# Performance work log

Hardware: AMD Instinct MI355X
Metric: run time of the kernel (lower is better)

The kernel has to match this reference:

```python
import jax, jax.numpy as jnp
import numpy as np

B, L, D = 16, 512, 128   # batch of sequences, seq len, input_dim
BN_EPS = 1e-5
TEMP = 1.0


def setup_inputs() -> dict:
    key = jax.random.key(0)
    ks = jax.random.split(key, 5)
    ids = jax.random.randint(ks[0], (B, L), 0, 50000)            # item ids per (seq, pos)
    log_mask = jnp.ones((B, L), dtype=jnp.int32)                 # all positions valid (static N)
    x1 = jax.random.normal(ks[1], (B * L, D), dtype=jnp.float32)
    x2 = jax.random.normal(ks[2], (B * L, D), dtype=jnp.float32)
    w1 = jax.random.normal(ks[3], (2 * D, D), dtype=jnp.float32) * 0.05  # torch Linear: [out, in]
    b1 = jnp.zeros((2 * D,), jnp.float32)
    w2 = jax.random.normal(ks[4], (D, 2 * D), dtype=jnp.float32) * 0.05
    b2 = jnp.zeros((D,), jnp.float32)
    gamma = jnp.ones((D,), jnp.float32)   # BatchNorm1d affine weight
    beta = jnp.zeros((D,), jnp.float32)   # BatchNorm1d affine bias
    return dict(ids=ids, log_mask=log_mask, x1=x1, x2=x2,
                w1=w1, b1=b1, w2=w2, b2=b2, gamma=gamma, beta=beta)


def _embed(x, w1, b1, w2, b2, gamma, beta):
    """linear1 -> relu -> linear2 -> BatchNorm1d (train-mode batch stats) -> L2 normalize."""
    h = jax.nn.relu(x @ w1.T + b1)
    y = h @ w2.T + b2
    mu = y.mean(axis=0)
    var = ((y - mu) ** 2).mean(axis=0)          # biased var, as torch BN uses for normalization
    y = (y - mu) * jax.lax.rsqrt(var + BN_EPS) * gamma + beta
    return y / jnp.linalg.norm(y, axis=1, keepdims=True)


def reference(ids, log_mask, x1, x2, w1, b1, w2, b2, gamma, beta):
    # log_mask is all-nonzero in this setup, so the gather by nonzero indices is the identity.
    nb, nl = ids.shape
    N = x1.shape[0]                      # = nb * nl valid anchors
    ids_f = ids.reshape(-1)
    seq = jnp.repeat(jnp.arange(nb), nl)  # seq_indexs: which sequence each row belongs to

    z1 = _embed(x1, w1, b1, w2, b2, gamma, beta)
    z2 = _embed(x2, w1, b1, w2, b2, gamma, beta)
    S = z1 @ z2.T                        # [N, N] cosine similarity (rows already unit-norm)

    idx = jnp.arange(N)
    ids_next = jnp.roll(ids_f, -1)
    seq_next = jnp.roll(seq, -1)
    # two-positive branch: i < N-1 and same sequence as the next row
    two = (idx < N - 1) & (seq == seq_next)            # [N] bool

    diag = jnp.diagonal(S)                             # cos(anchor_i, input2_i)
    s_next = S[idx, (idx + 1) % N]                     # cos(anchor_i, input2_{i+1})

    cols = idx[None, :]
    neg1 = ids_f[None, :] != ids_f[:, None]                                # single-pos negatives
    neg2 = neg1 & (ids_f[None, :] != ids_next[:, None]) & (seq[None, :] != seq[:, None])
    mask = jnp.where(two[:, None], neg2, neg1)
    # add the positives (self, and i+1 in the two-positive branch)
    mask = mask | (cols == idx[:, None]) | (two[:, None] & (cols == idx[:, None] + 1))

    denom = jnp.sum(jnp.where(mask, jnp.exp(S / TEMP), 0.0), axis=1)       # [N]
    pos_sum = diag + jnp.where(two, s_next, 0.0)
    n_pos = 1.0 + two.astype(S.dtype)

    inner = -(pos_sum / TEMP - jnp.log(denom)) / n_pos
    return jnp.sum(inner) / N
```

## Files before the change

### kernel.cpp

```cpp
#include <hip/hip_runtime.h>

#define N_TOT 8192
#define SEQ_L 512
#define D 128
#define NCHUNK 16
#define CHUNK (N_TOT / NCHUNK)
#define NJT (CHUNK / 64)
#define LOG2E 1.4426950408889634f
#define LN2   0.6931471805599453f

using bf16x8  = __attribute__((ext_vector_type(8))) short;
using f32x4   = __attribute__((ext_vector_type(4))) float;

static __device__ __forceinline__ unsigned short f2bf(float f) {
    unsigned int u = __float_as_uint(f);
    u = (u + 0x7FFFu + ((u >> 16) & 1u)) >> 16;
    return (unsigned short)u;
}
static __device__ __forceinline__ float bf2f(unsigned short h) {
    return __uint_as_float(((unsigned int)h) << 16);
}
static __device__ __forceinline__ float dot8(bf16x8 a, bf16x8 b) {
    float s = 0.f;
    #pragma unroll
    for (int k = 0; k < 8; ++k)
        s = fmaf(bf2f((unsigned short)a[k]), bf2f((unsigned short)b[k]), s);
    return s;
}

__global__ __launch_bounds__(256) void convert_w_kernel(
    const float* __restrict__ w1, const float* __restrict__ w2,
    unsigned short* __restrict__ w1b, unsigned short* __restrict__ w2b)
{
    int idx = blockIdx.x * 256 + threadIdx.x;
    const float* src = (idx < 8192) ? w1 : w2;
    unsigned short* dst = (idx < 8192) ? w1b : w2b;
    int off = ((idx < 8192) ? idx : idx - 8192) * 4;
    float4 v = *(const float4*)(src + off);
    ushort4 o;
    o.x = f2bf(v.x); o.y = f2bf(v.y); o.z = f2bf(v.z); o.w = f2bf(v.w);
    *(ushort4*)(dst + off) = o;
}

__global__ __launch_bounds__(256) void mlp_mfma_kernel(
    const float* __restrict__ x1, const float* __restrict__ x2,
    const unsigned short* __restrict__ w1b, const float* __restrict__ b1,
    const unsigned short* __restrict__ w2b, const float* __restrict__ b2,
    unsigned short* __restrict__ z1, unsigned short* __restrict__ z2,
    float* __restrict__ part_s, float* __restrict__ part_ss)
{
    __shared__ unsigned short hsh[32][264];
    const int t = threadIdx.x;
    const int w = t >> 6;
    const int lane = t & 63;
    const int g = lane >> 4;
    const int c16 = lane & 15;
    const int tensor = blockIdx.x >> 8;
    const int blk = blockIdx.x & 255;
    const int r0 = blk * 32;
    const float* __restrict__ x = tensor ? x2 : x1;
    unsigned short* __restrict__ z = tensor ? z2 : z1;

    bf16x8 af[2][4];
    #pragma unroll
    for (int rf = 0; rf < 2; ++rf)
        #pragma unroll
        for (int ks = 0; ks < 4; ++ks) {
            const float* xp = x + (size_t)(r0 + rf * 16 + c16) * D + ks * 32 + g * 8;
            float4 u0 = *(const float4*)xp;
            float4 u1 = *(const float4*)(xp + 4);
            bf16x8 a;
            a[0] = f2bf(u0.x); a[1] = f2bf(u0.y); a[2] = f2bf(u0.z); a[3] = f2bf(u0.w);
            a[4] = f2bf(u1.x); a[5] = f2bf(u1.y); a[6] = f2bf(u1.z); a[7] = f2bf(u1.w);
            af[rf][ks] = a;
        }
    f32x4 acc1[2][4] = {};
    #pragma unroll
    for (int ks = 0; ks < 4; ++ks)
        #pragma unroll
        for (int nf = 0; nf < 4; ++nf) {
            int n = w * 64 + nf * 16 + c16;
            bf16x8 b = *(const bf16x8*)(w1b + (size_t)n * D + ks * 32 + g * 8);
            #pragma unroll
            for (int rf = 0; rf < 2; ++rf)
                acc1[rf][nf] = __builtin_amdgcn_mfma_f32_16x16x32_bf16(af[rf][ks], b, acc1[rf][nf], 0, 0, 0);
        }
    #pragma unroll
    for (int nf = 0; nf < 4; ++nf) {
        float bb = b1[w * 64 + nf * 16 + c16];
        #pragma unroll
        for (int rf = 0; rf < 2; ++rf)
            #pragma unroll
            for (int r = 0; r < 4; ++r)
                hsh[rf * 16 + g * 4 + r][w * 64 + nf * 16 + c16] = f2bf(fmaxf(acc1[rf][nf][r] + bb, 0.f));
    }
    __syncthreads();

    f32x4 acc2[2][2] = {};
    #pragma unroll
    for (int ks = 0; ks < 8; ++ks) {
        bf16x8 a0 = *(const bf16x8*)(&hsh[c16][ks * 32 + g * 8]);
        bf16x8 a1 = *(const bf16x8*)(&hsh[16 + c16][ks * 32 + g * 8]);
        #pragma unroll
        for (int nf = 0; nf < 2; ++nf) {
            int n = w * 32 + nf * 16 + c16;
            bf16x8 b = *(const bf16x8*)(w2b + (size_t)n * 256 + ks * 32 + g * 8);
            acc2[0][nf] = __builtin_amdgcn_mfma_f32_16x16x32_bf16(a0, b, acc2[0][nf], 0, 0, 0);
            acc2[1][nf] = __builtin_amdgcn_mfma_f32_16x16x32_bf16(a1, b, acc2[1][nf], 0, 0, 0);
        }
    }

    #pragma unroll
    for (int nf = 0; nf < 2; ++nf) {
        int col = w * 32 + nf * 16 + c16;
        float bb = b2[col];
        float s = 0.f, ss = 0.f;
        #pragma unroll
        for (int rf = 0; rf < 2; ++rf)
            #pragma unroll
            for (int r = 0; r < 4; ++r) {
                float v = acc2[rf][nf][r] + bb;
                z[(size_t)(r0 + rf * 16 + g * 4 + r) * D + col] = f2bf(v);
                s += v; ss += v * v;
            }
        s  += __shfl_xor(s, 16);  s  += __shfl_xor(s, 32);
        ss += __shfl_xor(ss, 16); ss += __shfl_xor(ss, 32);
        if (g == 0) {
            part_s [((size_t)tensor * 256 + blk) * D + col] = s;
            part_ss[((size_t)tensor * 256 + blk) * D + col] = ss;
        }
    }
}

__global__ __launch_bounds__(256) void bn_reduce_kernel(
    const float* __restrict__ part_s, const float* __restrict__ part_ss,
    const float* __restrict__ gamma,
    float* __restrict__ mu, float* __restrict__ sc)
{
    const int t = threadIdx.x;
    const int tensor = blockIdx.x >> 7;
    const int col = blockIdx.x & 127;
    float s  = part_s [((size_t)tensor * 256 + t) * D + col];
    float ss = part_ss[((size_t)tensor * 256 + t) * D + col];
    #pragma unroll
    for (int m = 32; m; m >>= 1) { s += __shfl_xor(s, m); ss += __shfl_xor(ss, m); }
    __shared__ float rs[4], rss[4];
    if ((t & 63) == 0) { rs[t >> 6] = s; rss[t >> 6] = ss; }
    __syncthreads();
    if (t == 0) {
        float S = rs[0] + rs[1] + rs[2] + rs[3];
        float SS = rss[0] + rss[1] + rss[2] + rss[3];
        float m = S / (float)N_TOT;
        float var = SS / (float)N_TOT - m * m;
        mu[tensor * D + col] = m;
        sc[tensor * D + col] = gamma[col] * rsqrtf(var + 1e-5f);
    }
}

__global__ __launch_bounds__(256) void bn_l2_kernel(
    unsigned short* __restrict__ z1, unsigned short* __restrict__ z2,
    const float* __restrict__ mu, const float* __restrict__ sc,
    const float* __restrict__ beta)
{
    const int t = threadIdx.x;
    const int tensor = blockIdx.x >> 11;
    const int row = (blockIdx.x & 2047) * 4 + (t >> 6);
    const int lane = t & 63;
    unsigned short* __restrict__ yr = (tensor ? z2 : z1) + (size_t)row * D;
    const float* __restrict__ mub = mu + tensor * D;
    const float* __restrict__ scb = sc + tensor * D;

    ushort2 v = ((const ushort2*)yr)[lane];
    float2 m2 = ((const float2*)mub)[lane];
    float2 s2 = ((const float2*)scb)[lane];
    float2 b2 = ((const float2*)beta)[lane];
    float v0 = (bf2f(v.x) - m2.x) * s2.x + b2.x;
    float v1 = (bf2f(v.y) - m2.y) * s2.y + b2.y;
    float ssq = v0 * v0 + v1 * v1;
    #pragma unroll
    for (int m = 32; m; m >>= 1) ssq += __shfl_xor(ssq, m);
    float rn = rsqrtf(ssq);
    if (tensor == 0) rn *= LOG2E;
    ushort2 o; o.x = f2bf(v0 * rn); o.y = f2bf(v1 * rn);
    ((ushort2*)yr)[lane] = o;
}

__global__ __launch_bounds__(256) void diag_kernel(
    const short* __restrict__ z1, const short* __restrict__ z2,
    const int* __restrict__ ids,
    float* __restrict__ posv, float* __restrict__ dden)
{
    const int t = threadIdx.x;
    if (blockIdx.x < 256) {
        const int row = blockIdx.x * 32 + (t >> 3);
        const int le = t & 7;
        const short* ap = z1 + (size_t)row * D + le * 16;
        const short* bp = z2 + (size_t)row * D + le * 16;
        const short* cp = z2 + (size_t)((row + 1) & (N_TOT - 1)) * D + le * 16;
        bf16x8 a0 = *(const bf16x8*)ap, a1 = *(const bf16x8*)(ap + 8);
        float s1 = dot8(a0, *(const bf16x8*)bp) + dot8(a1, *(const bf16x8*)(bp + 8));
        float s2 = dot8(a0, *(const bf16x8*)cp) + dot8(a1, *(const bf16x8*)(cp + 8));
        #pragma unroll
        for (int m = 1; m < 8; m <<= 1) { s1 += __shfl_xor(s1, m); s2 += __shfl_xor(s2, m); }
        if (le == 0) {
            bool two = (row & (SEQ_L - 1)) != (SEQ_L - 1);
            if (two) {
                posv[row] = (s1 + s2) * LN2;
                dden[row] = exp2f(s1) + exp2f(s2);
            } else {
                posv[row] = s1 * LN2;
            }
        }
    } else {
        const int sr = blockIdx.x - 256;
        const int i = sr * SEQ_L + (SEQ_L - 1);
        const int jbase = sr * SEQ_L;
        const int idi_ = ids[i];
        float acc = 0.f;
        #pragma unroll
        for (int c = 0; c < 2; ++c) {
            int j = jbase + t * 2 + c;
            float s = 0.f;
            for (int k = 0; k < 16; ++k) {
                bf16x8 va = *(const bf16x8*)(z1 + (size_t)i * D + k * 8);
                bf16x8 vb = *(const bf16x8*)(z2 + (size_t)j * D + k * 8);
                s += dot8(va, vb);
            }
            bool m = (ids[j] != idi_) | (j == i);
            acc += m ? exp2f(s) : 0.f;
        }
        #pragma unroll
        for (int m = 32; m; m >>= 1) acc += __shfl_xor(acc, m);
        __shared__ float red[4];
        if ((t & 63) == 0) red[t >> 6] = acc;
        __syncthreads();
        if (t == 0) dden[i] = red[0] + red[1] + red[2] + red[3];
    }
}

__global__ __launch_bounds__(256, 2) void loss_mfma_kernel(
    const short* __restrict__ z1, const short* __restrict__ z2,
    const int* __restrict__ ids,
    float* __restrict__ den_part)
{
    const int t    = threadIdx.x;
    const int w    = t >> 6;
    const int lane = t & 63;
    const int g    = lane >> 4;
    const int c16  = lane & 15;

    const int c15 = blockIdx.x % 15;
    const int rbi = blockIdx.x / 15;
    const int rb  = rbi * 256;
    const int seqb = rb >> 9;
    const int chunk = c15 + (c15 >= seqb);
    const int jbase = chunk * CHUNK;

    const int i_wb = rb + w * 64;

    __shared__ __align__(16) unsigned char z2s[2][64 * 256];

    const int srow = t >> 2;
    const int sq   = t & 3;
    const int wxor = (srow & 7) << 4;
    const int rxor = (c16 & 7) << 4;

    bf16x8 af[4][4];
    #pragma unroll
    for (int rf = 0; rf < 4; ++rf)
        #pragma unroll
        for (int ks = 0; ks < 4; ++ks)
            af[rf][ks] = *(const bf16x8*)(z1 + (size_t)(i_wb + rf * 16 + c16) * D + ks * 32 + g * 8);

    int idi[4][4], idn_s[4][4];
    #pragma unroll
    for (int rf = 0; rf < 4; ++rf)
        #pragma unroll
        for (int r = 0; r < 4; ++r) {
            int i = i_wb + rf * 16 + g * 4 + r;
            idi[rf][r] = ids[i];
            bool tw = ((i & (SEQ_L - 1)) != (SEQ_L - 1));
            idn_s[rf][r] = tw ? ids[(i + 1) & (N_TOT - 1)] : idi[rf][r];
        }

    #pragma unroll
    for (int it = 0; it < 4; ++it) {
        bf16x8 v = *(const bf16x8*)(z2 + (size_t)(jbase + srow) * D + sq * 8 + it * 32);
        *(bf16x8*)&z2s[0][srow * 256 + ((sq * 16 + it * 64) ^ wxor)] = v;
    }
    __syncthreads();

    float den[4][4] = {};
    int cbuf = 0;

    #pragma unroll 1
    for (int jt = 0; jt < NJT; ++jt) {
        const int cb = jbase + jt * 64;

        bf16x8 stg[4];
        if (jt + 1 < NJT) {
            #pragma unroll
            for (int it = 0; it < 4; ++it)
                stg[it] = *(const bf16x8*)(z2 + (size_t)(cb + 64 + srow) * D + sq * 8 + it * 32);
        }

        int idj[4];
        #pragma unroll
        for (int nf = 0; nf < 4; ++nf) idj[nf] = ids[cb + nf * 16 + c16];

        f32x4 acc[4][4] = {};
        #pragma unroll
        for (int ks = 0; ks < 4; ++ks)
            #pragma unroll
            for (int nf = 0; nf < 4; ++nf) {
                bf16x8 b = *(const bf16x8*)&z2s[cbuf][(nf * 16 + c16) * 256 + ((ks * 64 + g * 16) ^ rxor)];
                #pragma unroll
                for (int rf = 0; rf < 4; ++rf)
                    acc[rf][nf] = __builtin_amdgcn_mfma_f32_16x16x32_bf16(af[rf][ks], b, acc[rf][nf], 0, 0, 0);
            }

        if (jt + 1 < NJT) {
            #pragma unroll
            for (int it = 0; it < 4; ++it)
                *(bf16x8*)&z2s[cbuf ^ 1][srow * 256 + ((sq * 16 + it * 64) ^ wxor)] = stg[it];
        }
        __syncthreads();

        #pragma unroll
        for (int rf = 0; rf < 4; ++rf)
            #pragma unroll
            for (int nf = 0; nf < 4; ++nf)
                #pragma unroll
                for (int r = 0; r < 4; ++r) {
                    float e = exp2f(acc[rf][nf][r]);
                    bool m = (idj[nf] != idi[rf][r]) & (idj[nf] != idn_s[rf][r]);
                    den[rf][r] += m ? e : 0.f;
                }
        cbuf ^= 1;
    }

    #pragma unroll
    for (int rf = 0; rf < 4; ++rf)
        #pragma unroll
        for (int r = 0; r < 4; ++r) {
            float dsum = den[rf][r];
            dsum += __shfl_xor(dsum, 1);
            dsum += __shfl_xor(dsum, 2);
            dsum += __shfl_xor(dsum, 4);
            dsum += __shfl_xor(dsum, 8);
            if (c16 == 0)
                den_part[chunk * N_TOT + i_wb + rf * 16 + g * 4 + r] = dsum;
        }
}

__global__ __launch_bounds__(1024) void loss_finish_kernel(
    const float* __restrict__ den_part, const float* __restrict__ posv,
    const float* __restrict__ dden, float* __restrict__ out)
{
    const int t = threadIdx.x;
    float v = 0.f;
    for (int k = 0; k < N_TOT / 1024; ++k) {
        int row = t + k * 1024;
        int seqb = row >> 9;
        float den = dden[row];
        #pragma unroll
        for (int q = 0; q < NCHUNK; ++q)
            if (q != seqb) den += den_part[q * N_TOT + row];
        bool two = ((row & (SEQ_L - 1)) != (SEQ_L - 1));
        float npos = two ? 2.f : 1.f;
        v += -(posv[row] - logf(den)) / npos;
    }
    #pragma unroll
    for (int m = 32; m; m >>= 1) v += __shfl_xor(v, m);
    __shared__ float red[16];
    if ((t & 63) == 0) red[t >> 6] = v;
    __syncthreads();
    if (t == 0) {
        float tot = 0.f;
        #pragma unroll
        for (int i = 0; i < 16; ++i) tot += red[i];
        out[0] = tot / (float)N_TOT;
    }
}

extern "C" void kernel_launch(void* const* d_in, const int* in_sizes, int n_in,
                              void* d_out, int out_size, void* d_ws, size_t ws_size,
                              hipStream_t stream)
{
    const int*   ids   = (const int*)d_in[0];
    const float* x1    = (const float*)d_in[2];
    const float* x2    = (const float*)d_in[3];
    const float* w1    = (const float*)d_in[4];
    const float* b1    = (const float*)d_in[5];
    const float* w2    = (const float*)d_in[6];
    const float* b2    = (const float*)d_in[7];
    const float* gamma = (const float*)d_in[8];
    const float* beta  = (const float*)d_in[9];

    char* ws = (char*)d_ws;
    unsigned short* z1b = (unsigned short*)ws;
    unsigned short* z2b = (unsigned short*)(ws + (2u << 20));
    float* part_s  = (float*)(ws + (4u << 20));
    float* part_ss = part_s + 2 * 256 * D;
    float* mu      = part_ss + 2 * 256 * D;
    float* sc      = mu + 2 * D;
    float* den_part = sc + 2 * D;
    float* posv    = den_part + NCHUNK * N_TOT;
    float* dden    = posv + N_TOT;
    unsigned short* w1b = (unsigned short*)(dden + N_TOT);
    unsigned short* w2b = w1b + 256 * D;

    convert_w_kernel<<<64, 256, 0, stream>>>(w1, w2, w1b, w2b);
    mlp_mfma_kernel<<<512, 256, 0, stream>>>(x1, x2, w1b, b1, w2b, b2,
                                             z1b, z2b, part_s, part_ss);
    bn_reduce_kernel<<<256, 256, 0, stream>>>(part_s, part_ss, gamma, mu, sc);
    bn_l2_kernel<<<4096, 256, 0, stream>>>(z1b, z2b, mu, sc, beta);
    diag_kernel<<<272, 256, 0, stream>>>((const short*)z1b, (const short*)z2b,
                                         ids, posv, dden);
    loss_mfma_kernel<<<480, 256, 0, stream>>>((const short*)z1b, (const short*)z2b,
                                              ids, den_part);
    loss_finish_kernel<<<1, 1024, 0, stream>>>(den_part, posv, dden, (float*)d_out);
}
```

Baseline: 87.02 us.

## Merge diag and loss kernels, split column chunks, widen BN-L2 rows per wave

The diagonal/positive kernel and the MFMA denominator kernel are merged into one launch, and the branch is picked by block index. Each off-diagonal chunk is split into two halves, doubling the loss grid to 960 blocks, which adds parallelism and shortens each block's tile loop. bn_l2 now processes two rows per wave with 4-element vector accesses, halving its grid. In exchange, the per-chunk partials buffer doubles and the finish kernel reads twice as many partial sums.

```diff
diff --git a/kernel.cpp b/kernel.cpp
--- a/kernel.cpp
+++ b/kernel.cpp
@@ -5,7 +5,8 @@
 #define D 128
 #define NCHUNK 16
 #define CHUNK (N_TOT / NCHUNK)
-#define NJT (CHUNK / 64)
+#define NJT_H 4
+#define NDIAG 272
 #define LOG2E 1.4426950408889634f
 #define LN2   0.6931471805599453f
 
@@ -163,36 +164,45 @@
     const float* __restrict__ beta)
 {
     const int t = threadIdx.x;
-    const int tensor = blockIdx.x >> 11;
-    const int row = (blockIdx.x & 2047) * 4 + (t >> 6);
+    const int wv = t >> 6;
     const int lane = t & 63;
-    unsigned short* __restrict__ yr = (tensor ? z2 : z1) + (size_t)row * D;
-    const float* __restrict__ mub = mu + tensor * D;
-    const float* __restrict__ scb = sc + tensor * D;
-
-    ushort2 v = ((const ushort2*)yr)[lane];
-    float2 m2 = ((const float2*)mub)[lane];
-    float2 s2 = ((const float2*)scb)[lane];
-    float2 b2 = ((const float2*)beta)[lane];
-    float v0 = (bf2f(v.x) - m2.x) * s2.x + b2.x;
-    float v1 = (bf2f(v.y) - m2.y) * s2.y + b2.y;
-    float ssq = v0 * v0 + v1 * v1;
-    #pragma unroll
-    for (int m = 32; m; m >>= 1) ssq += __shfl_xor(ssq, m);
+    const int rw = lane >> 5;
+    const int cl = lane & 31;
+    const int grow = blockIdx.x * 8 + wv * 2 + rw;
+    const int tensor = grow >> 13;
+    const int row = grow & (N_TOT - 1);
+
+    unsigned short* __restrict__ yr = (tensor ? z2 : z1) + (size_t)row * D + cl * 4;
+    float4 m4 = *(const float4*)(mu + tensor * D + cl * 4);
+    float4 s4 = *(const float4*)(sc + tensor * D + cl * 4);
+    float4 b4 = *(const float4*)(beta + cl * 4);
+    ushort4 v = *(const ushort4*)yr;
+    float v0 = (bf2f(v.x) - m4.x) * s4.x + b4.x;
+    float v1 = (bf2f(v.y) - m4.y) * s4.y + b4.y;
+    float v2 = (bf2f(v.z) - m4.z) * s4.z + b4.z;
+    float v3 = (bf2f(v.w) - m4.w) * s4.w + b4.w;
+    float ssq = v0 * v0 + v1 * v1 + v2 * v2 + v3 * v3;
+    #pragma unroll
+    for (int m = 16; m; m >>= 1) ssq += __shfl_xor(ssq, m);
     float rn = rsqrtf(ssq);
     if (tensor == 0) rn *= LOG2E;
-    ushort2 o; o.x = f2bf(v0 * rn); o.y = f2bf(v1 * rn);
-    ((ushort2*)yr)[lane] = o;
-}
-
-__global__ __launch_bounds__(256) void diag_kernel(
+    ushort4 o;
+    o.x = f2bf(v0 * rn); o.y = f2bf(v1 * rn);
+    o.z = f2bf(v2 * rn); o.w = f2bf(v3 * rn);
+    *(ushort4*)yr = o;
+}
+
+__global__ __launch_bounds__(256, 2) void loss_all_kernel(
     const short* __restrict__ z1, const short* __restrict__ z2,
     const int* __restrict__ ids,
-    float* __restrict__ posv, float* __restrict__ dden)
+    float* __restrict__ posv, float* __restrict__ dden,
+    float* __restrict__ den_part)
 {
     const int t = threadIdx.x;
-    if (blockIdx.x < 256) {
-        const int row = blockIdx.x * 32 + (t >> 3);
+    const int bid = blockIdx.x;
+
+    if (bid < 256) {
+        const int row = bid * 32 + (t >> 3);
         const int le = t & 7;
         const short* ap = z1 + (size_t)row * D + le * 16;
         const short* bp = z2 + (size_t)row * D + le * 16;
@@ -211,8 +221,11 @@
                 posv[row] = s1 * LN2;
             }
         }
-    } else {
-        const int sr = blockIdx.x - 256;
+        return;
+    }
+    if (bid < NDIAG) {
+        __shared__ float red[4];
+        const int sr = bid - 256;
         const int i = sr * SEQ_L + (SEQ_L - 1);
         const int jbase = sr * SEQ_L;
         const int idi_ = ids[i];
@@ -231,30 +244,26 @@
         }
         #pragma unroll
         for (int m = 32; m; m >>= 1) acc += __shfl_xor(acc, m);
-        __shared__ float red[4];
         if ((t & 63) == 0) red[t >> 6] = acc;
         __syncthreads();
         if (t == 0) dden[i] = red[0] + red[1] + red[2] + red[3];
-    }
-}
-
-__global__ __launch_bounds__(256, 2) void loss_mfma_kernel(
-    const short* __restrict__ z1, const short* __restrict__ z2,
-    const int* __restrict__ ids,
-    float* __restrict__ den_part)
-{
-    const int t    = threadIdx.x;
+        return;
+    }
+
+    const int bidm = bid - NDIAG;
     const int w    = t >> 6;
     const int lane = t & 63;
     const int g    = lane >> 4;
     const int c16  = lane & 15;
 
-    const int c15 = blockIdx.x % 15;
-    const int rbi = blockIdx.x / 15;
-    const int rb  = rbi * 256;
+    const int c15  = bidm % 15;
+    const int rbh  = bidm / 15;
+    const int rbi  = rbh >> 1;
+    const int half = rbh & 1;
+    const int rb   = rbi * 256;
     const int seqb = rb >> 9;
     const int chunk = c15 + (c15 >= seqb);
-    const int jbase = chunk * CHUNK;
+    const int jbase = chunk * CHUNK + half * 256;
 
     const int i_wb = rb + w * 64;
 
@@ -294,11 +303,11 @@
     int cbuf = 0;
 
     #pragma unroll 1
-    for (int jt = 0; jt < NJT; ++jt) {
+    for (int jt = 0; jt < NJT_H; ++jt) {
         const int cb = jbase + jt * 64;
 
         bf16x8 stg[4];
-        if (jt + 1 < NJT) {
+        if (jt + 1 < NJT_H) {
             #pragma unroll
             for (int it = 0; it < 4; ++it)
                 stg[it] = *(const bf16x8*)(z2 + (size_t)(cb + 64 + srow) * D + sq * 8 + it * 32);
@@ -319,7 +328,7 @@
                     acc[rf][nf] = __builtin_amdgcn_mfma_f32_16x16x32_bf16(af[rf][ks], b, acc[rf][nf], 0, 0, 0);
             }
 
-        if (jt + 1 < NJT) {
+        if (jt + 1 < NJT_H) {
             #pragma unroll
             for (int it = 0; it < 4; ++it)
                 *(bf16x8*)&z2s[cbuf ^ 1][srow * 256 + ((sq * 16 + it * 64) ^ wxor)] = stg[it];
@@ -349,7 +358,7 @@
             dsum += __shfl_xor(dsum, 4);
             dsum += __shfl_xor(dsum, 8);
             if (c16 == 0)
-                den_part[chunk * N_TOT + i_wb + rf * 16 + g * 4 + r] = dsum;
+                den_part[(chunk * 2 + half) * N_TOT + i_wb + rf * 16 + g * 4 + r] = dsum;
         }
 }
 
@@ -364,8 +373,8 @@
         int seqb = row >> 9;
         float den = dden[row];
         #pragma unroll
-        for (int q = 0; q < NCHUNK; ++q)
-            if (q != seqb) den += den_part[q * N_TOT + row];
+        for (int q = 0; q < 2 * NCHUNK; ++q)
+            if ((q >> 1) != seqb) den += den_part[q * N_TOT + row];
         bool two = ((row & (SEQ_L - 1)) != (SEQ_L - 1));
         float npos = two ? 2.f : 1.f;
         v += -(posv[row] - logf(den)) / npos;
@@ -405,7 +414,7 @@
     float* mu      = part_ss + 2 * 256 * D;
     float* sc      = mu + 2 * D;
     float* den_part = sc + 2 * D;
-    float* posv    = den_part + NCHUNK * N_TOT;
+    float* posv    = den_part + 2 * NCHUNK * N_TOT;
     float* dden    = posv + N_TOT;
     unsigned short* w1b = (unsigned short*)(dden + N_TOT);
     unsigned short* w2b = w1b + 256 * D;
@@ -414,10 +423,8 @@
     mlp_mfma_kernel<<<512, 256, 0, stream>>>(x1, x2, w1b, b1, w2b, b2,
                                              z1b, z2b, part_s, part_ss);
     bn_reduce_kernel<<<256, 256, 0, stream>>>(part_s, part_ss, gamma, mu, sc);
-    bn_l2_kernel<<<4096, 256, 0, stream>>>(z1b, z2b, mu, sc, beta);
-    diag_kernel<<<272, 256, 0, stream>>>((const short*)z1b, (const short*)z2b,
-                                         ids, posv, dden);
-    loss_mfma_kernel<<<480, 256, 0, stream>>>((const short*)z1b, (const short*)z2b,
-                                              ids, den_part);
+    bn_l2_kernel<<<2048, 256, 0, stream>>>(z1b, z2b, mu, sc, beta);
+    loss_all_kernel<<<NDIAG + 960, 256, 0, stream>>>((const short*)z1b, (const short*)z2b,
+                                                     ids, posv, dden, den_part);
     loss_finish_kernel<<<1, 1024, 0, stream>>>(den_part, posv, dden, (float*)d_out);
 }
```

After: 143.6 us. 1.65x slower.
